# Kernel optimization log

Measured on AMD Instinct MI355X. Metric: run time of the kernel, lower is better.

Reference implementation:

```python
import jax, jax.numpy as jnp
import numpy as np

HEAD_SIZE = 128
NUM_EMBED = 1024
BLOCK_SIZE = 2048


def setup_inputs() -> dict:
    key = jax.random.key(0)
    kx, kk, kq, kv = jax.random.split(key, 4)
    x = jax.random.normal(kx, (4, BLOCK_SIZE, NUM_EMBED), dtype=jnp.float32)
    s = 1.0 / np.sqrt(NUM_EMBED)
    Wk = jax.random.normal(kk, (NUM_EMBED, HEAD_SIZE), dtype=jnp.float32) * s
    Wq = jax.random.normal(kq, (NUM_EMBED, HEAD_SIZE), dtype=jnp.float32) * s
    Wv = jax.random.normal(kv, (NUM_EMBED, HEAD_SIZE), dtype=jnp.float32) * s
    return {"x": x, "Wk": Wk, "Wq": Wq, "Wv": Wv}


def reference(x, Wk, Wq, Wv):
    # x: [B, T, C]; W*: [C, H]
    B, T, C = x.shape
    k = x @ Wk          # [B, T, H]
    q = x @ Wq          # [B, T, H]
    v = x @ Wv          # [B, T, H]
    scale = k.shape[-1] ** -0.5
    wei = jnp.einsum('bth,bsh->bts', q, k) * scale  # [B, T, T]
    causal = jnp.tril(jnp.ones((T, T), dtype=bool))
    wei = jnp.where(causal, wei, -jnp.inf)
    wei = jax.nn.softmax(wei, axis=-1)
    out = jnp.einsum('bts,bsh->bth', wei, v)        # [B, T, H]
    return out
```

## Files before the change

kernel.cpp:

```cpp
#include <hip/hip_runtime.h>
#include <hip/hip_bf16.h>
#include <math.h>

#define B_ 4
#define T_ 2048
#define C_ 1024
#define H_ 128
#define SCALE 0.088388347648318447f

typedef unsigned short u16;
typedef __bf16 bf16x8 __attribute__((ext_vector_type(8)));
typedef __bf16 bf16x4 __attribute__((ext_vector_type(4)));
typedef float  f32x4  __attribute__((ext_vector_type(4)));
typedef u16    u16x8  __attribute__((ext_vector_type(8)));
typedef u16    u16x4  __attribute__((ext_vector_type(4)));

#define PO_OFF  0u
#define ML_OFF  18874368u
#define WBT_OFF 19169280u
#define QB_OFF  19955712u
#define KB_OFF  22052864u
#define VT_OFF  24150016u

__device__ __forceinline__ u16 f2bf(float f) {
    __hip_bfloat16 h = __float2bfloat16(f);
    return __builtin_bit_cast(u16, h);
}

__device__ __forceinline__ void load_lds16(const void* g, void* l) {
    __builtin_amdgcn_global_load_lds(
        (const __attribute__((address_space(1))) unsigned int*)g,
        (__attribute__((address_space(3))) unsigned int*)l, 16, 0, 0);
}

__global__ __launch_bounds__(256) void convert_w(const float* __restrict__ Wq,
                                                 const float* __restrict__ Wk,
                                                 const float* __restrict__ Wv,
                                                 u16* __restrict__ wbT) {
    const int id = blockIdx.x * 256 + threadIdx.x;
    const int s = id >> 17;
    const int r = id & 131071;
    const int k = r >> 7, n = r & 127;
    const float* W = (s == 0) ? Wq : (s == 1) ? Wk : Wv;
    float v = W[k * 128 + n];
    if (s == 0) v *= SCALE;
    wbT[(s << 17) + (n << 10) + k] = f2bf(v);
}

__global__ __launch_bounds__(256) void gemm_qkv(
    const float* __restrict__ x, const u16* __restrict__ wbT,
    u16* __restrict__ qb, u16* __restrict__ kb, u16* __restrict__ vT)
{
    __shared__ u16 xs[2][2048];
    __shared__ u16 ws[2][8192];

    const int tid = threadIdx.x;
    const int w = tid >> 6, lane = tid & 63, lg = lane >> 4, lr = lane & 15;
    const int wm = w >> 1, wn = w & 1;
    const int s = blockIdx.y;
    const int m0 = blockIdx.x * 32;
    const u16* wsrc = wbT + (s << 17);

    const int xrow = tid >> 3;
    const int xseg = tid & 7;
    const float* xbase = x + (size_t)(m0 + xrow) * C_ + xseg * 8;
    const unsigned xsw = ((unsigned)xrow & 7u) << 4;

    unsigned wro[4], wco[4];
#pragma unroll
    for (int i = 0; i < 4; ++i) {
        const unsigned o = (unsigned)(w * 4 + i) * 1024u + (unsigned)lane * 16u;
        const unsigned o2 = o ^ (((o >> 7) & 7u) << 4);
        wro[i] = o2 >> 7; wco[i] = (o2 & 127u) >> 1;
    }

    f32x4 acc[4] = {};

    {
        const float4 f0 = ((const float4*)xbase)[0], f1 = ((const float4*)xbase)[1];
#pragma unroll
        for (int i = 0; i < 4; ++i)
            load_lds16(wsrc + (size_t)wro[i] * C_ + wco[i], &ws[0][(w * 4 + i) * 512]);
        u16x8 pk;
        pk[0] = f2bf(f0.x); pk[1] = f2bf(f0.y); pk[2] = f2bf(f0.z); pk[3] = f2bf(f0.w);
        pk[4] = f2bf(f1.x); pk[5] = f2bf(f1.y); pk[6] = f2bf(f1.z); pk[7] = f2bf(f1.w);
        *(u16x8*)((char*)xs[0] + xrow * 128 + (((unsigned)xseg * 16) ^ xsw)) = pk;
    }
    __syncthreads();

    int buf = 0;
    for (int k0 = 0; k0 < C_; k0 += 64) {
        const bool pf = (k0 + 64 < C_);
        float4 g0, g1;
        if (pf) {
            const float* xn = xbase + k0 + 64;
            g0 = ((const float4*)xn)[0]; g1 = ((const float4*)xn)[1];
#pragma unroll
            for (int i = 0; i < 4; ++i)
                load_lds16(wsrc + (size_t)wro[i] * C_ + (k0 + 64) + wco[i],
                           &ws[buf ^ 1][(w * 4 + i) * 512]);
        }

        const int arow = wm * 16 + lr;
        const unsigned asw = ((unsigned)arow & 7u) << 4;
#pragma unroll
        for (int kc = 0; kc < 2; ++kc) {
            const unsigned kb_ = (unsigned)(kc * 64 + lg * 16);
            const bf16x8 af = *(const bf16x8*)((const char*)xs[buf] + arow * 128 + (kb_ ^ asw));
            bf16x8 bfr[4];
#pragma unroll
            for (int ni = 0; ni < 4; ++ni) {
                const int n = wn * 64 + ni * 16 + lr;
                bfr[ni] = *(const bf16x8*)((const char*)ws[buf] + n * 128 + (kb_ ^ (((unsigned)n & 7u) << 4)));
            }
#pragma unroll
            for (int ni = 0; ni < 4; ++ni)
                acc[ni] = __builtin_amdgcn_mfma_f32_16x16x32_bf16(af, bfr[ni], acc[ni], 0, 0, 0);
        }

        if (pf) {
            u16x8 pk;
            pk[0] = f2bf(g0.x); pk[1] = f2bf(g0.y); pk[2] = f2bf(g0.z); pk[3] = f2bf(g0.w);
            pk[4] = f2bf(g1.x); pk[5] = f2bf(g1.y); pk[6] = f2bf(g1.z); pk[7] = f2bf(g1.w);
            *(u16x8*)((char*)xs[buf ^ 1] + xrow * 128 + (((unsigned)xseg * 16) ^ xsw)) = pk;
        }
        __syncthreads();
        buf ^= 1;
    }

    if (s < 2) {
        u16* dst = (s == 0) ? qb : kb;
#pragma unroll
        for (int ni = 0; ni < 4; ++ni) {
            const int trow = m0 + wm * 16 + lg * 4;
            const int col = wn * 64 + ni * 16 + lr;
#pragma unroll
            for (int r = 0; r < 4; ++r)
                dst[(size_t)(trow + r) * H_ + col] = f2bf(acc[ni][r]);
        }
    } else {
#pragma unroll
        for (int ni = 0; ni < 4; ++ni) {
            const int trow = m0 + wm * 16 + lg * 4;
            const int bb = trow >> 11, t = trow & 2047;
            const int d = wn * 64 + ni * 16 + lr;
            u16x4 pk;
            pk[0] = f2bf(acc[ni][0]); pk[1] = f2bf(acc[ni][1]);
            pk[2] = f2bf(acc[ni][2]); pk[3] = f2bf(acc[ni][3]);
            *(u16x4*)&vT[((size_t)bb * 128 + d) * 2048 + t] = pk;
        }
    }
}

__global__ __launch_bounds__(256) void attn_split(
    const u16* __restrict__ qb, const u16* __restrict__ kb,
    const u16* __restrict__ vT, float* __restrict__ po, float* __restrict__ ml)
{
    __shared__ u16 ks[2][4096];
    __shared__ u16 vs[2][128 * 36];

    const int jt = blockIdx.x, sp = blockIdx.y, b = blockIdx.z;
    const int kt0 = sp * 8;
    const int ktend_all = 2 * jt + 2;
    if (kt0 >= ktend_all) return;
    const int kt_end = min(kt0 + 8, ktend_all);

    const int tid = threadIdx.x;
    const int w = tid >> 6, lane = tid & 63, lg = lane >> 4, lr = lane & 15;
    const int qrow_base = jt * 64 + w * 16;

    const u16* kbB = kb + ((size_t)(b << 11)) * H_;
    const u16* vbB = vT + (size_t)b * 128 * 2048;

    unsigned krow[2], kcolb[2];
#pragma unroll
    for (int i = 0; i < 2; ++i) {
        const unsigned o_ = (unsigned)(w * 2 + i) * 1024u + (unsigned)lane * 16u;
        const unsigned o2 = o_ ^ (((o_ >> 8) & 7u) << 4);
        krow[i] = o2 >> 8; kcolb[i] = o2 & 255u;
    }
    int vd[2], vc[2];
#pragma unroll
    for (int i = 0; i < 2; ++i) {
        const int idx = i * 256 + tid;
        vd[i] = idx >> 2; vc[i] = idx & 3;
    }

    const u16* qp = qb + ((size_t)(b << 11) + qrow_base + lr) * H_;
    bf16x8 qf[4];
#pragma unroll
    for (int kc = 0; kc < 4; ++kc)
        qf[kc] = *(const bf16x8*)&qp[kc * 32 + lg * 8];

    u16x8 vr[2];
    {
        const u16* kbase = kbB + (size_t)kt0 * 32 * H_;
#pragma unroll
        for (int i = 0; i < 2; ++i)
            load_lds16((const char*)kbase + krow[i] * 256 + kcolb[i], &ks[0][(w * 2 + i) * 512]);
        const u16* vbase = vbB + (size_t)kt0 * 32;
#pragma unroll
        for (int i = 0; i < 2; ++i)
            vr[i] = *(const u16x8*)&vbase[(size_t)vd[i] * 2048 + vc[i] * 8];
#pragma unroll
        for (int i = 0; i < 2; ++i) {
            char* rb = (char*)vs[0] + vd[i] * 72 + (vc[i] & 2) * 4;
            *(u16x4*)(rb + ((2 * vc[i]) & 3) * 16)     = __builtin_shufflevector(vr[i], vr[i], 0, 1, 2, 3);
            *(u16x4*)(rb + ((2 * vc[i] + 1) & 3) * 16) = __builtin_shufflevector(vr[i], vr[i], 4, 5, 6, 7);
        }
    }
    __syncthreads();

    f32x4 o[8] = {};
    float m_run = -1e30f, l_run = 0.f;
    int cur = 0;

    for (int kt = kt0; kt < kt_end; ++kt) {
        const bool pf = (kt + 1 < kt_end);
        if (pf) {
            const u16* kbase = kbB + (size_t)(kt + 1) * 32 * H_;
#pragma unroll
            for (int i = 0; i < 2; ++i)
                load_lds16((const char*)kbase + krow[i] * 256 + kcolb[i],
                           &ks[cur ^ 1][(w * 2 + i) * 512]);
            const u16* vbase = vbB + (size_t)(kt + 1) * 32;
#pragma unroll
            for (int i = 0; i < 2; ++i)
                vr[i] = *(const u16x8*)&vbase[(size_t)vd[i] * 2048 + vc[i] * 8];
        }

        f32x4 s0 = {0.f, 0.f, 0.f, 0.f}, s1 = {0.f, 0.f, 0.f, 0.f};
        const unsigned swz = ((unsigned)lr & 7u) << 4;
#pragma unroll
        for (int kc = 0; kc < 4; ++kc) {
            const unsigned byte = ((unsigned)(kc * 64 + lg * 16)) ^ swz;
            const bf16x8 kf0 = *(const bf16x8*)((const char*)ks[cur] + lr * 256 + byte);
            const bf16x8 kf1 = *(const bf16x8*)((const char*)ks[cur] + lr * 256 + 4096 + byte);
            s0 = __builtin_amdgcn_mfma_f32_16x16x32_bf16(kf0, qf[kc], s0, 0, 0, 0);
            s1 = __builtin_amdgcn_mfma_f32_16x16x32_bf16(kf1, qf[kc], s1, 0, 0, 0);
        }

        if (kt * 32 + 31 > qrow_base) {
            const int qg = qrow_base + lr;
            const int kvb = kt * 32 + lg * 4;
#pragma unroll
            for (int r = 0; r < 4; ++r) {
                if (kvb + r > qg)      s0[r] = -INFINITY;
                if (kvb + 16 + r > qg) s1[r] = -INFINITY;
            }
        }

        float mt = fmaxf(fmaxf(fmaxf(s0[0], s0[1]), fmaxf(s0[2], s0[3])),
                         fmaxf(fmaxf(s1[0], s1[1]), fmaxf(s1[2], s1[3])));
        mt = fmaxf(mt, __shfl_xor(mt, 16));
        mt = fmaxf(mt, __shfl_xor(mt, 32));
        if (__any(mt > m_run + 8.f)) {
            const float mn = fmaxf(m_run, mt);
            const float f = __expf(m_run - mn);
            const float fb0 = __shfl(f, lg * 4 + 0);
            const float fb1 = __shfl(f, lg * 4 + 1);
            const float fb2 = __shfl(f, lg * 4 + 2);
            const float fb3 = __shfl(f, lg * 4 + 3);
#pragma unroll
            for (int ni = 0; ni < 8; ++ni) {
                o[ni][0] *= fb0; o[ni][1] *= fb1; o[ni][2] *= fb2; o[ni][3] *= fb3;
            }
            l_run *= f;
            m_run = mn;
        }
        const float p0 = __expf(s0[0] - m_run), p1 = __expf(s0[1] - m_run);
        const float p2 = __expf(s0[2] - m_run), p3 = __expf(s0[3] - m_run);
        const float p4 = __expf(s1[0] - m_run), p5 = __expf(s1[1] - m_run);
        const float p6 = __expf(s1[2] - m_run), p7 = __expf(s1[3] - m_run);
        float sum = ((p0 + p1) + (p2 + p3)) + ((p4 + p5) + (p6 + p7));
        sum += __shfl_xor(sum, 16);
        sum += __shfl_xor(sum, 32);
        l_run += sum;

        bf16x8 pa;
        pa[0] = (__bf16)p0; pa[1] = (__bf16)p1; pa[2] = (__bf16)p2; pa[3] = (__bf16)p3;
        pa[4] = (__bf16)p4; pa[5] = (__bf16)p5; pa[6] = (__bf16)p6; pa[7] = (__bf16)p7;

#pragma unroll
        for (int ni = 0; ni < 8; ++ni) {
            const bf16x8 vf = *(const bf16x8*)((const char*)vs[cur] + (ni * 16 + lr) * 72 + lg * 16);
            o[ni] = __builtin_amdgcn_mfma_f32_16x16x32_bf16(pa, vf, o[ni], 0, 0, 0);
        }

        if (pf) {
#pragma unroll
            for (int i = 0; i < 2; ++i) {
                char* rb = (char*)vs[cur ^ 1] + vd[i] * 72 + (vc[i] & 2) * 4;
                *(u16x4*)(rb + ((2 * vc[i]) & 3) * 16)     = __builtin_shufflevector(vr[i], vr[i], 0, 1, 2, 3);
                *(u16x4*)(rb + ((2 * vc[i] + 1) & 3) * 16) = __builtin_shufflevector(vr[i], vr[i], 4, 5, 6, 7);
            }
        }
        __syncthreads();
        cur ^= 1;
    }

    const int a = jt >> 2, b3 = jt & 3;
    const int slot = (a + 1) * (2 * a + b3) + sp;
    float* pob = po + (size_t)(b * 144 + slot) * 64 * 128;
#pragma unroll
    for (int ni = 0; ni < 8; ++ni) {
        const int col = ni * 16 + lr;
#pragma unroll
        for (int rj = 0; rj < 4; ++rj)
            pob[(w * 16 + lg * 4 + rj) * 128 + col] = o[ni][rj];
    }
    if (lg == 0) {
        float* mlb = ml + (size_t)(b * 144 + slot) * 128;
        mlb[w * 16 + lr] = m_run;
        mlb[64 + w * 16 + lr] = l_run;
    }
}

__global__ __launch_bounds__(256) void attn_combine(
    const float* __restrict__ po, const float* __restrict__ ml,
    float* __restrict__ out)
{
    const int rid = (blockIdx.x << 3) + (threadIdx.x >> 5);
    const int b = blockIdx.y;
    const int d4 = (threadIdx.x & 31) * 4;
    const int jt = rid >> 6, row = rid & 63;
    const int a = jt >> 2, b3 = jt & 3;
    const int slot0 = (a + 1) * (2 * a + b3);
    const int c = a + 1;

    float M = -INFINITY;
#pragma unroll
    for (int si = 0; si < 8; ++si)
        if (si < c) M = fmaxf(M, ml[(size_t)(b * 144 + slot0 + si) * 128 + row]);

    float L = 0.f;
    float a0 = 0.f, a1 = 0.f, a2 = 0.f, a3 = 0.f;
#pragma unroll
    for (int si = 0; si < 8; ++si) {
        if (si < c) {
            const float* mlb = ml + (size_t)(b * 144 + slot0 + si) * 128;
            const float wgt = __expf(mlb[row] - M);
            L += wgt * mlb[64 + row];
            const float4 t = *(const float4*)&po[((size_t)(b * 144 + slot0 + si) * 64 + row) * 128 + d4];
            a0 = fmaf(wgt, t.x, a0); a1 = fmaf(wgt, t.y, a1);
            a2 = fmaf(wgt, t.z, a2); a3 = fmaf(wgt, t.w, a3);
        }
    }
    const float inv = 1.f / L;
    *(float4*)&out[((size_t)(b << 11) + rid) * H_ + d4] =
        make_float4(a0 * inv, a1 * inv, a2 * inv, a3 * inv);
}

extern "C" void kernel_launch(void* const* d_in, const int* in_sizes, int n_in,
                              void* d_out, int out_size, void* d_ws, size_t ws_size,
                              hipStream_t stream) {
    const float* x  = (const float*)d_in[0];
    const float* Wk = (const float*)d_in[1];
    const float* Wq = (const float*)d_in[2];
    const float* Wv = (const float*)d_in[3];
    float* out = (float*)d_out;

    float* po = (float*)((char*)d_ws + PO_OFF);
    float* ml = (float*)((char*)d_ws + ML_OFF);
    u16* wbT  = (u16*)((char*)d_ws + WBT_OFF);
    u16* qb   = (u16*)((char*)d_ws + QB_OFF);
    u16* kb   = (u16*)((char*)d_ws + KB_OFF);
    u16* vT   = (u16*)((char*)d_ws + VT_OFF);

    convert_w<<<1536, 256, 0, stream>>>(Wq, Wk, Wv, wbT);
    gemm_qkv<<<dim3(256, 3), 256, 0, stream>>>(x, wbT, qb, kb, vT);
    attn_split<<<dim3(32, 8, 4), 256, 0, stream>>>(qb, kb, vT, po, ml);
    attn_combine<<<dim3(256, 4), 256, 0, stream>>>(po, ml, out);
}
```

Baseline: 64.16 us.

## Fuse Q, K, V projections into one GEMM block sharing x tile

The QKV projection kernel now computes all three outputs in one block instead of launching a separate grid slice per projection. Each x tile is loaded and converted to bf16 once and reused against all three weight slices, which cuts redundant fp32 x reads from global memory by a factor of three. In exchange, LDS per block grows to about 104KB, there are three times as many accumulators, and the grid drops from 768 to 256 blocks. That lowers occupancy and parallelism on a device with many compute units.

```diff
diff --git a/kernel.cpp b/kernel.cpp
--- a/kernel.cpp
+++ b/kernel.cpp
@@ -47,40 +47,44 @@
     wbT[(s << 17) + (n << 10) + k] = f2bf(v);
 }
 
-__global__ __launch_bounds__(256) void gemm_qkv(
+__global__ __launch_bounds__(256) void gemm_qkv3(
     const float* __restrict__ x, const u16* __restrict__ wbT,
     u16* __restrict__ qb, u16* __restrict__ kb, u16* __restrict__ vT)
 {
     __shared__ u16 xs[2][2048];
-    __shared__ u16 ws[2][8192];
+    __shared__ u16 ws[2][24576];
 
     const int tid = threadIdx.x;
     const int w = tid >> 6, lane = tid & 63, lg = lane >> 4, lr = lane & 15;
     const int wm = w >> 1, wn = w & 1;
-    const int s = blockIdx.y;
     const int m0 = blockIdx.x * 32;
-    const u16* wsrc = wbT + (s << 17);
 
     const int xrow = tid >> 3;
     const int xseg = tid & 7;
     const float* xbase = x + (size_t)(m0 + xrow) * C_ + xseg * 8;
     const unsigned xsw = ((unsigned)xrow & 7u) << 4;
 
-    unsigned wro[4], wco[4];
-#pragma unroll
-    for (int i = 0; i < 4; ++i) {
-        const unsigned o = (unsigned)(w * 4 + i) * 1024u + (unsigned)lane * 16u;
+    const u16* wsrcp[12];
+    unsigned wdst[12];
+#pragma unroll
+    for (int i = 0; i < 12; ++i) {
+        const int cc = w * 12 + i;
+        const int s3 = cc >> 4;
+        const int c16 = cc & 15;
+        const unsigned o = (unsigned)c16 * 1024u + (unsigned)lane * 16u;
         const unsigned o2 = o ^ (((o >> 7) & 7u) << 4);
-        wro[i] = o2 >> 7; wco[i] = (o2 & 127u) >> 1;
-    }
-
-    f32x4 acc[4] = {};
+        const unsigned row = o2 >> 7, col = (o2 & 127u) >> 1;
+        wsrcp[i] = wbT + (s3 << 17) + (size_t)row * C_ + col;
+        wdst[i] = s3 * 8192 + c16 * 512;
+    }
+
+    f32x4 acc[3][4] = {};
 
     {
         const float4 f0 = ((const float4*)xbase)[0], f1 = ((const float4*)xbase)[1];
 #pragma unroll
-        for (int i = 0; i < 4; ++i)
-            load_lds16(wsrc + (size_t)wro[i] * C_ + wco[i], &ws[0][(w * 4 + i) * 512]);
+        for (int i = 0; i < 12; ++i)
+            load_lds16(wsrcp[i], &ws[0][wdst[i]]);
         u16x8 pk;
         pk[0] = f2bf(f0.x); pk[1] = f2bf(f0.y); pk[2] = f2bf(f0.z); pk[3] = f2bf(f0.w);
         pk[4] = f2bf(f1.x); pk[5] = f2bf(f1.y); pk[6] = f2bf(f1.z); pk[7] = f2bf(f1.w);
@@ -88,65 +92,68 @@
     }
     __syncthreads();
 
-    int buf = 0;
-    for (int k0 = 0; k0 < C_; k0 += 64) {
-        const bool pf = (k0 + 64 < C_);
+#pragma unroll 1
+    for (int j = 0; j < 16; ++j) {
+        const int k0 = j * 64;
+        const bool pf = (j + 1 < 16);
         float4 g0, g1;
         if (pf) {
+#pragma unroll
+            for (int i = 0; i < 12; ++i)
+                load_lds16(wsrcp[i] + k0 + 64, &ws[(j + 1) & 1][wdst[i]]);
             const float* xn = xbase + k0 + 64;
             g0 = ((const float4*)xn)[0]; g1 = ((const float4*)xn)[1];
-#pragma unroll
-            for (int i = 0; i < 4; ++i)
-                load_lds16(wsrc + (size_t)wro[i] * C_ + (k0 + 64) + wco[i],
-                           &ws[buf ^ 1][(w * 4 + i) * 512]);
-        }
-
+        }
+
+        const u16* xsb = xs[j & 1];
+        const char* wsb = (const char*)ws[j & 1];
         const int arow = wm * 16 + lr;
         const unsigned asw = ((unsigned)arow & 7u) << 4;
 #pragma unroll
         for (int kc = 0; kc < 2; ++kc) {
             const unsigned kb_ = (unsigned)(kc * 64 + lg * 16);
-            const bf16x8 af = *(const bf16x8*)((const char*)xs[buf] + arow * 128 + (kb_ ^ asw));
-            bf16x8 bfr[4];
-#pragma unroll
-            for (int ni = 0; ni < 4; ++ni) {
-                const int n = wn * 64 + ni * 16 + lr;
-                bfr[ni] = *(const bf16x8*)((const char*)ws[buf] + n * 128 + (kb_ ^ (((unsigned)n & 7u) << 4)));
+            const bf16x8 af = *(const bf16x8*)((const char*)xsb + arow * 128 + (kb_ ^ asw));
+#pragma unroll
+            for (int s3 = 0; s3 < 3; ++s3) {
+#pragma unroll
+                for (int ni = 0; ni < 4; ++ni) {
+                    const int n = wn * 64 + ni * 16 + lr;
+                    const bf16x8 bfr = *(const bf16x8*)(wsb + s3 * 16384 + n * 128 +
+                                                        (kb_ ^ (((unsigned)n & 7u) << 4)));
+                    acc[s3][ni] = __builtin_amdgcn_mfma_f32_16x16x32_bf16(af, bfr, acc[s3][ni], 0, 0, 0);
+                }
             }
-#pragma unroll
-            for (int ni = 0; ni < 4; ++ni)
-                acc[ni] = __builtin_amdgcn_mfma_f32_16x16x32_bf16(af, bfr[ni], acc[ni], 0, 0, 0);
         }
 
         if (pf) {
             u16x8 pk;
             pk[0] = f2bf(g0.x); pk[1] = f2bf(g0.y); pk[2] = f2bf(g0.z); pk[3] = f2bf(g0.w);
             pk[4] = f2bf(g1.x); pk[5] = f2bf(g1.y); pk[6] = f2bf(g1.z); pk[7] = f2bf(g1.w);
-            *(u16x8*)((char*)xs[buf ^ 1] + xrow * 128 + (((unsigned)xseg * 16) ^ xsw)) = pk;
+            *(u16x8*)((char*)xs[(j + 1) & 1] + xrow * 128 + (((unsigned)xseg * 16) ^ xsw)) = pk;
         }
         __syncthreads();
-        buf ^= 1;
-    }
-
-    if (s < 2) {
-        u16* dst = (s == 0) ? qb : kb;
+    }
+
+    const int trow = m0 + wm * 16 + lg * 4;
+#pragma unroll
+    for (int s3 = 0; s3 < 2; ++s3) {
+        u16* dst = (s3 == 0) ? qb : kb;
 #pragma unroll
         for (int ni = 0; ni < 4; ++ni) {
-            const int trow = m0 + wm * 16 + lg * 4;
             const int col = wn * 64 + ni * 16 + lr;
 #pragma unroll
             for (int r = 0; r < 4; ++r)
-                dst[(size_t)(trow + r) * H_ + col] = f2bf(acc[ni][r]);
-        }
-    } else {
+                dst[(size_t)(trow + r) * H_ + col] = f2bf(acc[s3][ni][r]);
+        }
+    }
+    {
+        const int bb = trow >> 11, t = trow & 2047;
 #pragma unroll
         for (int ni = 0; ni < 4; ++ni) {
-            const int trow = m0 + wm * 16 + lg * 4;
-            const int bb = trow >> 11, t = trow & 2047;
             const int d = wn * 64 + ni * 16 + lr;
             u16x4 pk;
-            pk[0] = f2bf(acc[ni][0]); pk[1] = f2bf(acc[ni][1]);
-            pk[2] = f2bf(acc[ni][2]); pk[3] = f2bf(acc[ni][3]);
+            pk[0] = f2bf(acc[2][ni][0]); pk[1] = f2bf(acc[2][ni][1]);
+            pk[2] = f2bf(acc[2][ni][2]); pk[3] = f2bf(acc[2][ni][3]);
             *(u16x4*)&vT[((size_t)bb * 128 + d) * 2048 + t] = pk;
         }
     }
@@ -368,7 +375,7 @@
     u16* vT   = (u16*)((char*)d_ws + VT_OFF);
 
     convert_w<<<1536, 256, 0, stream>>>(Wq, Wk, Wv, wbT);
-    gemm_qkv<<<dim3(256, 3), 256, 0, stream>>>(x, wbT, qb, kb, vT);
+    gemm_qkv3<<<256, 256, 0, stream>>>(x, wbT, qb, kb, vT);
     attn_split<<<dim3(32, 8, 4), 256, 0, stream>>>(qb, kb, vT, po, ml);
     attn_combine<<<dim3(256, 4), 256, 0, stream>>>(po, ml, out);
 }
```

Result: slower. 76.30 us (+18.9%).
